# Kernel tuning notes

Hardware: AMD Instinct MI355X
Metric: run time of the kernel (lower is better)

The kernel has to match this reference:

```python
import jax, jax.numpy as jnp
import numpy as np

TIMESTEPS = 8
TAU = 1.0
DELTA_T = 0.05
ALPHA = 0.3
VTH_BOUND = 0.0005
BATCH, C, H, W = 32, 128, 32, 32


def setup_inputs() -> dict:
    key = jax.random.key(0)
    x = jax.random.normal(key, (TIMESTEPS * BATCH, C, H, W), dtype=jnp.float32)
    Vth = jnp.asarray(1.0, dtype=jnp.float32)
    return {"x": x, "Vth": Vth}


def reference(x, Vth):
    # no-grad Vth clamp from LIFNeuron.forward: relu(Vth - bound) + bound
    Vth = jax.nn.relu(Vth - VTH_BOUND) + VTH_BOUND
    chw = x.shape[1:]
    xr = x.reshape(TIMESTEPS, -1, *chw)            # [T, B, C, H, W]
    beta = jnp.exp(jnp.asarray(-DELTA_T / TAU, x.dtype))

    def step(mem, xt):
        mem = beta * mem + (1.0 - beta) * xt       # leaky integrate
        spike = (mem >= ALPHA * Vth).astype(x.dtype) * Vth
        return mem - spike, spike / DELTA_T        # reset by subtraction

    mem0 = jnp.zeros(xr.shape[1:], dtype=x.dtype)
    _, spikes = jax.lax.scan(step, mem0, xr)       # spikes: [T, B, C, H, W]
    return spikes.reshape(x.shape)                 # torch.cat(spikes, 0)
```

## Files before the change

### kernel.cpp

```cpp
#include <hip/hip_runtime.h>


#define T_STEPS 8
#define S_ELEMS (32 * 128 * 32 * 32)
#define S4 (S_ELEMS / 4)
#define BLOCK 256
#define K_COLS 8
#define GRID (S4 / (BLOCK * K_COLS))

typedef float f32x4 __attribute__((ext_vector_type(4)));

__global__ __launch_bounds__(BLOCK) void lif_fwd_kernel(
    const f32x4* __restrict__ x, const float* __restrict__ vth_ptr,
    f32x4* __restrict__ out) {
  const int base = blockIdx.x * (BLOCK * K_COLS) + threadIdx.x;

  const float vth_raw = vth_ptr[0];
  const float vth = __fadd_rn(fmaxf(__fsub_rn(vth_raw, 0.0005f), 0.0f), 0.0005f);
  const float thr = __fmul_rn(0.3f, vth);
  const float outval = __fdiv_rn(vth, 0.05f);

  const float beta = 0x1.E7078Cp-1f;
  const float omb = __fsub_rn(1.0f, beta);

  float m[K_COLS * 4];
#pragma unroll
  for (int j = 0; j < K_COLS * 4; ++j) m[j] = 0.0f;

#pragma unroll
  for (int t = 0; t < T_STEPS; ++t) {
    const size_t p = (size_t)t * S4;

    f32x4 xv[K_COLS];
#pragma unroll
    for (int k = 0; k < K_COLS; ++k) xv[k] = x[base + k * BLOCK + p];

#pragma unroll
    for (int k = 0; k < K_COLS; ++k) {
      f32x4 o;
#pragma unroll
      for (int c = 0; c < 4; ++c) {
        const float mm =
            __fadd_rn(__fmul_rn(beta, m[k * 4 + c]), __fmul_rn(omb, xv[k][c]));
        const bool s = (mm >= thr);
        o[c] = s ? outval : 0.0f;
        m[k * 4 + c] = s ? __fsub_rn(mm, vth) : mm;
      }
      out[base + k * BLOCK + p] = o;
    }
  }
}

extern "C" void kernel_launch(void* const* d_in, const int* in_sizes, int n_in,
                              void* d_out, int out_size, void* d_ws,
                              size_t ws_size, hipStream_t stream) {
  const f32x4* x = (const f32x4*)d_in[0];
  const float* vth = (const float*)d_in[1];
  f32x4* out = (f32x4*)d_out;
  lif_fwd_kernel<<<GRID, BLOCK, 0, stream>>>(x, vth, out);
}
```

Measured before the change: 228.3 us.

## Stream inputs through double-buffered LDS with direct global-to-LDS loads

The kernel now loads input timesteps with global_load_lds straight into a per-wave, double-buffered LDS region. Explicit s_waitcnt vmcnt counts keep the next chunk's eight timestep loads in flight while the current chunk runs the LIF recurrence and writes its spikes. Each thread now walks 8 chunks of one f32x4 column in sequence instead of holding 8 columns in registers. This is meant to raise memory-level parallelism and cut register pressure. The cost is 64KB of LDS per block, and correctness depends on hand-counted vmcnt values that include the outstanding stores.

```diff
diff --git a/kernel.cpp b/kernel.cpp
--- a/kernel.cpp
+++ b/kernel.cpp
@@ -5,15 +5,30 @@
 #define S_ELEMS (32 * 128 * 32 * 32)
 #define S4 (S_ELEMS / 4)
 #define BLOCK 256
-#define K_COLS 8
-#define GRID (S4 / (BLOCK * K_COLS))
+#define W_PER_B 4
+#define ITERS 8
+#define CHUNK4 256
+#define BSPAN (CHUNK4 * ITERS)
+#define GRID (S4 / BSPAN)
 
 typedef float f32x4 __attribute__((ext_vector_type(4)));
 
-__global__ __launch_bounds__(BLOCK) void lif_fwd_kernel(
+#define WAITV(n) asm volatile("s_waitcnt vmcnt(" #n ")" ::: "memory")
+
+__device__ __forceinline__ void gload_lds16(const void* g, void* l) {
+  __builtin_amdgcn_global_load_lds(
+      (const __attribute__((address_space(1))) void*)g,
+      (__attribute__((address_space(3))) void*)l, 16, 0, 0);
+}
+
+__global__ __launch_bounds__(BLOCK) void lif_fwd_r14(
     const f32x4* __restrict__ x, const float* __restrict__ vth_ptr,
     f32x4* __restrict__ out) {
-  const int base = blockIdx.x * (BLOCK * K_COLS) + threadIdx.x;
+  __shared__ f32x4 lds4[4096];
+
+  const int tid = threadIdx.x;
+  const int lane = tid & 63;
+  const int w = __builtin_amdgcn_readfirstlane(tid >> 6);
 
   const float vth_raw = vth_ptr[0];
   const float vth = __fadd_rn(fmaxf(__fsub_rn(vth_raw, 0.0005f), 0.0f), 0.0005f);
@@ -23,32 +38,62 @@
   const float beta = 0x1.E7078Cp-1f;
   const float omb = __fsub_rn(1.0f, beta);
 
-  float m[K_COLS * 4];
+  const int bbase = blockIdx.x * BSPAN;
+
+  f32x4* const lw[2] = {&lds4[w * 1024], &lds4[w * 1024 + 512]};
+
+  auto issue8 = [&](int it, f32x4* lbuf) {
+    const f32x4* gp = x + (size_t)(bbase + it * CHUNK4 + w * 64 + lane);
 #pragma unroll
-  for (int j = 0; j < K_COLS * 4; ++j) m[j] = 0.0f;
+    for (int t = 0; t < T_STEPS; ++t) {
+      gload_lds16(gp + (size_t)t * S4, lbuf + t * 64);
+    }
+  };
 
+  auto compute8 = [&](int it, const f32x4* lbuf) {
+    const size_t gbase = (size_t)(bbase + it * CHUNK4 + w * 64 + lane);
+    float m0 = 0.0f, m1 = 0.0f, m2 = 0.0f, m3 = 0.0f;
 #pragma unroll
-  for (int t = 0; t < T_STEPS; ++t) {
-    const size_t p = (size_t)t * S4;
+    for (int t = 0; t < T_STEPS; ++t) {
+      const f32x4 xv = lbuf[t * 64 + lane];
+      f32x4 o;
+      {
+        const float mm = __fadd_rn(__fmul_rn(beta, m0), __fmul_rn(omb, xv[0]));
+        const bool s = (mm >= thr);
+        o[0] = s ? outval : 0.0f;
+        m0 = s ? __fsub_rn(mm, vth) : mm;
+      }
+      {
+        const float mm = __fadd_rn(__fmul_rn(beta, m1), __fmul_rn(omb, xv[1]));
+        const bool s = (mm >= thr);
+        o[1] = s ? outval : 0.0f;
+        m1 = s ? __fsub_rn(mm, vth) : mm;
+      }
+      {
+        const float mm = __fadd_rn(__fmul_rn(beta, m2), __fmul_rn(omb, xv[2]));
+        const bool s = (mm >= thr);
+        o[2] = s ? outval : 0.0f;
+        m2 = s ? __fsub_rn(mm, vth) : mm;
+      }
+      {
+        const float mm = __fadd_rn(__fmul_rn(beta, m3), __fmul_rn(omb, xv[3]));
+        const bool s = (mm >= thr);
+        o[3] = s ? outval : 0.0f;
+        m3 = s ? __fsub_rn(mm, vth) : mm;
+      }
+      out[gbase + (size_t)t * S4] = o;
+    }
+  };
 
-    f32x4 xv[K_COLS];
-#pragma unroll
-    for (int k = 0; k < K_COLS; ++k) xv[k] = x[base + k * BLOCK + p];
-
-#pragma unroll
-    for (int k = 0; k < K_COLS; ++k) {
-      f32x4 o;
-#pragma unroll
-      for (int c = 0; c < 4; ++c) {
-        const float mm =
-            __fadd_rn(__fmul_rn(beta, m[k * 4 + c]), __fmul_rn(omb, xv[k][c]));
-        const bool s = (mm >= thr);
-        o[c] = s ? outval : 0.0f;
-        m[k * 4 + c] = s ? __fsub_rn(mm, vth) : mm;
-      }
-      out[base + k * BLOCK + p] = o;
-    }
-  }
+  issue8(0, lw[0]);
+  issue8(1, lw[1]); WAITV(8);  compute8(0, lw[0]);
+  issue8(2, lw[0]); WAITV(16); compute8(1, lw[1]);
+  issue8(3, lw[1]); WAITV(16); compute8(2, lw[0]);
+  issue8(4, lw[0]); WAITV(16); compute8(3, lw[1]);
+  issue8(5, lw[1]); WAITV(16); compute8(4, lw[0]);
+  issue8(6, lw[0]); WAITV(16); compute8(5, lw[1]);
+  issue8(7, lw[1]); WAITV(16); compute8(6, lw[0]);
+                    WAITV(8);  compute8(7, lw[1]);
 }
 
 extern "C" void kernel_launch(void* const* d_in, const int* in_sizes, int n_in,
@@ -57,5 +102,5 @@
   const f32x4* x = (const f32x4*)d_in[0];
   const float* vth = (const float*)d_in[1];
   f32x4* out = (f32x4*)d_out;
-  lif_fwd_kernel<<<GRID, BLOCK, 0, stream>>>(x, vth, out);
+  lif_fwd_r14<<<GRID, BLOCK, 0, stream>>>(x, vth, out);
 }
```

Result: slower. 238.9 us (+4.6%).
